# Kernel tuning notes

Measured on AMD Instinct MI355X. Metric: run time of the kernel, lower is better.

Reference implementation:

```python
import jax, jax.numpy as jnp
import numpy as np


def _gen_grid(h, w, stride=1):
    """Normalized spherical sampling grid, shape (3*H', 3*W', 2) with (x, y) order,
    matching gen_grid_coordinates in the torch source (vectorized)."""
    pi = np.pi
    dphi = pi / h
    dth = 2 * pi / w
    t = np.tan(dth)
    p = np.tan(dphi)
    sp = p / np.cos(dth)
    # xys[kr, kc] = (x, y) tangent-plane offsets of the 3x3 kernel taps
    xys = np.array([[[-t, sp], [0.0, p], [t, sp]],
                    [[-t, 0.0], [1.0, 1.0], [t, 0.0]],
                    [[-t, -sp], [0.0, -p], [t, -sp]]], dtype=np.float64)
    X = xys[..., 0]
    Y = xys[..., 1]
    rho = np.sqrt(X ** 2 + Y ** 2)           # [3,3], nonzero everywhere
    v = np.arctan(rho)
    rr = np.arange(0, h, stride)
    cc = np.arange(0, w, stride)
    phi = -((rr + 0.5) / h * pi - pi / 2)    # [H']
    theta = (cc + 0.5) / w * 2 * pi - pi     # [W']
    sphi = np.sin(phi)[:, None, None, None]  # [H',1,1,1]
    cphi = np.cos(phi)[:, None, None, None]
    arg = np.cos(v) * sphi + Y * np.sin(v) * cphi / rho  # [H',1,3,3]
    new_phi = np.arcsin(np.clip(arg, -1.0, 1.0))
    new_theta = theta[None, :, None, None] + np.arctan(
        X * np.sin(v) / (rho * cphi * np.cos(v) - Y * sphi * np.sin(v)))  # [H',W',3,3]
    new_r = np.broadcast_to((-new_phi + pi / 2) * h / pi - 0.5, new_theta.shape).copy()
    new_c = (new_theta + pi) * w / (2 * pi) - 0.5
    new_c = (new_c + w) % w
    # center tap samples the pixel itself
    new_r[:, :, 1, 1] = rr[:, None]
    new_c[:, :, 1, 1] = cc[None, :]
    gx = new_c * 2 / w - 1
    gy = new_r * 2 / h - 1
    grid = np.stack([gx, gy], axis=-1)                     # [H',W',3,3,2]
    Hp, Wp = len(rr), len(cc)
    grid = grid.transpose(0, 2, 1, 3, 4).reshape(Hp * 3, Wp * 3, 2)
    return grid.astype(np.float32)


def _grid_sample_bilinear_zeros(x, grid):
    """torch grid_sample(mode='bilinear', padding_mode='zeros', align_corners=False).
    x: [N,C,H,W]; grid: [Hg,Wg,2] (shared over batch). Returns [N,C,Hg,Wg]."""
    N, C, H, W = x.shape
    ix = ((grid[..., 0] + 1) * W - 1) * 0.5
    iy = ((grid[..., 1] + 1) * H - 1) * 0.5
    x0 = jnp.floor(ix)
    y0 = jnp.floor(iy)
    x1 = x0 + 1
    y1 = y0 + 1
    wx1 = ix - x0
    wx0 = 1.0 - wx1
    wy1 = iy - y0
    wy0 = 1.0 - wy1

    def gather(yy, xx):
        valid = ((xx >= 0) & (xx <= W - 1) & (yy >= 0) & (yy <= H - 1)).astype(x.dtype)
        xi = jnp.clip(xx, 0, W - 1).astype(jnp.int32)
        yi = jnp.clip(yy, 0, H - 1).astype(jnp.int32)
        return x[:, :, yi, xi], valid  # [N,C,Hg,Wg], [Hg,Wg]

    v00, m00 = gather(y0, x0)
    v01, m01 = gather(y0, x1)
    v10, m10 = gather(y1, x0)
    v11, m11 = gather(y1, x1)
    return (v00 * (wy0 * wx0 * m00) + v01 * (wy0 * wx1 * m01)
            + v10 * (wy1 * wx0 * m10) + v11 * (wy1 * wx1 * m11))


def setup_inputs() -> dict:
    key = jax.random.key(0)
    k1, k2, k3 = jax.random.split(key, 3)
    N, Cin, H, W = 4, 64, 128, 256
    Cout = 128
    x = jax.random.normal(k1, (N, Cin, H, W), dtype=jnp.float32)
    fan_in = Cin * 9
    bound = 1.0 / np.sqrt(fan_in)
    weight = jax.random.uniform(k2, (Cout, Cin, 3, 3), dtype=jnp.float32,
                                minval=-bound, maxval=bound)
    bias = jnp.zeros((Cout,), dtype=jnp.float32)
    return {"x": x, "weight": weight, "bias": bias}


def reference(x, weight, bias):
    H, W = int(x.shape[2]), int(x.shape[3])
    grid = jnp.asarray(_gen_grid(H, W, 1))              # [3H, 3W, 2]
    s = _grid_sample_bilinear_zeros(x, grid)            # [N, Cin, 3H, 3W]
    y = jax.lax.conv_general_dilated(
        s, weight, window_strides=(3, 3), padding='VALID',
        dimension_numbers=('NCHW', 'OIHW', 'NCHW'))     # [N, Cout, H, W]
    return y + bias[None, :, None, None]
```

## Files before the change

### kernel.cpp

```cpp
#include <hip/hip_runtime.h>
#include <math.h>

typedef __attribute__((ext_vector_type(8))) _Float16 half8;
typedef __attribute__((ext_vector_type(4))) _Float16 half4;
typedef __attribute__((ext_vector_type(2))) _Float16 half2;
typedef __attribute__((ext_vector_type(4))) float floatx4;
typedef __attribute__((ext_vector_type(4))) unsigned int uintx4;

#define NB    4
#define CIN   64
#define COUT  128
#define IMH   128
#define IMW   256
#define KTOT  576
#define NPIX  (IMH * IMW)
#define PXT   128
#define NDPB  (PXT * 9)
#define ROWS  4
#define CSTW  6
#define NCOL  257
#define RSTW  (NCOL * CSTW)
#define KCH   96

__device__ __forceinline__ unsigned pkrtz2(float a, float b) {
  unsigned r;
  asm("v_cvt_pkrtz_f16_f32 %0, %1, %2" : "=v"(r) : "v"(a), "v"(b));
  return r;
}
__device__ __forceinline__ half4 bcl(unsigned u) {
  half2 h; __builtin_memcpy(&h, &u, 4);
  return __builtin_shufflevector(h, h, 0, 0, 0, 0);
}
__device__ __forceinline__ half4 bch(unsigned u) {
  half2 h; __builtin_memcpy(&h, &u, 4);
  return __builtin_shufflevector(h, h, 1, 1, 1, 1);
}

__global__ __launch_bounds__(256) void prep_w_kernel(const float* __restrict__ w,
                                                     unsigned short* __restrict__ wbf) {
  int idx = blockIdx.x * 256 + threadIdx.x;
  if (idx >= COUT * 8 * KCH) return;
  int co = idx / (8 * KCH);
  int K2 = idx - co * (8 * KCH);
  int cb = K2 / KCH, kk = K2 - cb * KCH;
  unsigned short v = 0;
  if (kk < 72) {
    int t = kk >> 3, chl = kk & 7;
    int ci = cb * 8 + chl;
    _Float16 h = (_Float16)w[co * KTOT + ci * 9 + t];
    __builtin_memcpy(&v, &h, 2);
  }
  wbf[(K2 >> 3) * (COUT * 8) + co * 8 + (K2 & 7)] = v;
}

__global__ __launch_bounds__(512, 4) void sphconv_kernel(
    const float* __restrict__ x, const unsigned short* __restrict__ wbf,
    const float* __restrict__ bias, float* __restrict__ out) {
  __shared__ __align__(16) unsigned int stg[2][ROWS * RSTW];
  __shared__ __align__(16) unsigned int descL[12 * PXT * 4];
  __shared__ double tapA[9];
  __shared__ float  tapWy[9][2];
  __shared__ int    tapRo[9][2];

  const int tid  = threadIdx.x;
  const int lane = tid & 63;
  const int wv   = tid >> 6;
  const int lin = blockIdx.x + 2 * blockIdx.y;
  const int sw  = (lin & 7) * 32 + (lin >> 3);
  const int ct  = sw >> 7;
  const int r   = sw & 127;
  const int n   = blockIdx.z;
  const int c0  = ct * PXT;
  const int co_base = (wv & 1) * 64;
  const int px_base = (wv >> 1) * 32;
  const int rlo  = min(max(r - 2, 0), IMH - ROWS);
  const int q    = lane >> 4;
  const int p    = lane & 15;
  const int sp  = tid & 3;
  const int scg = (tid >> 2) & 63;
  const int srr = tid >> 8;

  const float* xn = x + (size_t)n * CIN * NPIX;

  floatx4 nx[4];
  #pragma unroll
  for (int c = 0; c < 2; c++)
    #pragma unroll
    for (int rw = 0; rw < 2; rw++)
      nx[c * 2 + rw] = *(const floatx4*)(xn + (size_t)(sp * 2 + c) * NPIX
                                         + (size_t)(rlo + srr * 2 + rw) * IMW + scg * 4);

  {
    int myk = -1;
    if (lane == 0) myk = wv;
    if (wv == 0 && lane == 32) myk = 8;
    if (myk >= 0) {
      const double pi = 3.14159265358979323846;
      double dphi = pi / IMH;
      double dth  = 2.0 * pi / IMW;
      double t  = tan(dth);
      double pp = tan(dphi);
      double sp_ = pp / cos(dth);
      double phi  = -(((double)r + 0.5) / IMH * pi - pi * 0.5);
      double sphi = sin(phi), cphi = cos(phi);
      int i = myk / 3, j = myk % 3;
      double atv, new_r;
      if (myk == 4) {
        atv = 0.0; new_r = (double)r;
      } else {
        double X = (j == 0) ? -t : ((j == 2) ? t : 0.0);
        double Y = 0.0;
        if (i == 0)      Y = (j == 1) ?  pp :  sp_;
        else if (i == 2) Y = (j == 1) ? -pp : -sp_;
        double rho = sqrt(X * X + Y * Y);
        double v   = atan(rho);
        double sv = sin(v), cv = cos(v);
        double arg = cv * sphi + Y * sv * cphi / rho;
        arg = fmin(1.0, fmax(-1.0, arg));
        double new_phi = asin(arg);
        double denom = rho * cphi * cv - Y * sphi * sv;
        atv = atan(X * sv / denom);
        new_r = (-new_phi + pi * 0.5) * IMH / pi - 0.5;
      }
      float gy = (float)(new_r * 2.0 / IMH - 1.0);
      float iy = ((gy + 1.0f) * (float)IMH - 1.0f) * 0.5f;
      float fy = floorf(iy); int y0 = (int)fy;
      float wy1 = iy - fy, wy0 = 1.0f - wy1;
      int y1 = y0 + 1;
      bool vy0 = (y0 >= 0) & (y0 <= IMH - 1);
      bool vy1 = (y1 >= 0) & (y1 <= IMH - 1);
      int y0c = min(max(y0, 0), IMH - 1), y1c = min(max(y1, 0), IMH - 1);
      int rt = min(max(y0c - rlo, 0), ROWS - 1);
      int rb = min(max(y1c - rlo, 0), ROWS - 1);
      tapA[myk] = atv;
      tapWy[myk][0] = vy0 ? wy0 : 0.0f;
      tapWy[myk][1] = vy1 ? wy1 : 0.0f;
      tapRo[myk][0] = rt * RSTW;
      tapRo[myk][1] = rb * RSTW;
    }
  }
  __syncthreads();

  {
    const double pi = 3.14159265358979323846;
    #pragma unroll
    for (int dd = 0; dd < 3; dd++) {
      if (dd < 2 || tid < NDPB - 1024) {
        int d  = tid + dd * 512;
        int px = d & (PXT - 1), k = d >> 7;
        int c  = c0 + px;
        double nc;
        if (k == 4) {
          nc = (double)c;
        } else {
          double theta = ((double)c + 0.5) / IMW * (2.0 * pi) - pi;
          double new_theta = theta + tapA[k];
          nc = (new_theta + pi) * IMW / (2.0 * pi) - 0.5;
          nc = fmod(nc + (double)IMW, (double)IMW);
        }
        float gx = (float)(nc * 2.0 / IMW - 1.0);
        float ix = ((gx + 1.0f) * (float)IMW - 1.0f) * 0.5f;
        float fx = floorf(ix); int x0 = (int)fx;
        float wx1 = ix - fx, wx0 = 1.0f - wx1;
        int x1 = x0 + 1;
        int x0c = max(x0, 0);
        float w_lo = (x0 >= 0) ? wx0 : wx1;
        float w_hi = (x0 >= 0) ? ((x1 <= IMW - 1) ? wx1 : 0.0f) : 0.0f;
        float wy0m = tapWy[k][0], wy1m = tapWy[k][1];
        int sh0 = ((x0c >> 4) & 1) * 2;
        int sh1 = (((x0c + 1) >> 4) & 1) * 2;
        int dc  = CSTW + sh1 - sh0;
        int offt = tapRo[k][0] + x0c * CSTW + sh0;
        int offb = tapRo[k][1] + x0c * CSTW + sh0;
        uintx4 rec;
        rec.x = (unsigned)(offt | (offb << 16));
        rec.y = pkrtz2(wy0m * w_lo, wy0m * w_hi);
        rec.z = pkrtz2(wy1m * w_lo, wy1m * w_hi);
        rec.w = (unsigned)dc;
        *(uintx4*)&descL[(k * PXT + px) * 4] = rec;
      }
    }
  }
  if (tid < 3 * PXT) {
    uintx4 zr = {0u, 0u, 0u, (unsigned)CSTW};
    *(uintx4*)&descL[((9 + (tid >> 7)) * PXT + (tid & (PXT - 1))) * 4] = zr;
  }

  #pragma unroll
  for (int rw = 0; rw < 2; rw++)
    #pragma unroll
    for (int i = 0; i < 4; i++) {
      int col = scg * 4 + i;
      int sh = ((col >> 4) & 1) * 2;
      stg[0][(srr * 2 + rw) * RSTW + col * CSTW + sh + sp] =
          pkrtz2(nx[rw][i], nx[2 + rw][i]);
    }
  if (tid < 32) stg[tid >> 4][((tid >> 2) & 3) * RSTW + 256 * CSTW + (tid & 3)] = 0u;

  floatx4 acc[4][2];
  #pragma unroll
  for (int mt = 0; mt < 4; mt++)
    #pragma unroll
    for (int nt = 0; nt < 2; nt++)
      acc[mt][nt] = (floatx4){0.f, 0.f, 0.f, 0.f};

  __syncthreads();

  #pragma unroll 1
  for (int cb = 0; cb < 8; cb++) {
    if (cb < 7) {
      #pragma unroll
      for (int c = 0; c < 2; c++)
        #pragma unroll
        for (int rw = 0; rw < 2; rw++)
          nx[c * 2 + rw] = *(const floatx4*)(xn + (size_t)((cb + 1) * 8 + sp * 2 + c) * NPIX
                                             + (size_t)(rlo + srr * 2 + rw) * IMW + scg * 4);
    }
    const unsigned int* sb = &stg[cb & 1][0];
    #pragma unroll
    for (int nt = 0; nt < 2; nt++) {
      const int pxl = px_base + nt * 16 + p;
      #pragma unroll
      for (int ks = 0; ks < 3; ks++) {
        uintx4 rec = *(const uintx4*)&descL[((ks * 4 + q) * PXT + pxl) * 4];
        unsigned op = rec.x;
        int dc = (int)rec.w;
        const unsigned int* pt = sb + (op & 0xFFFFu);
        const unsigned int* pb = sb + (op >> 16);
        half4 t0  = *(const half4*)(pt);
        half4 t0h = *(const half4*)(pt + 2);
        half4 t1  = *(const half4*)(pt + dc);
        half4 t1h = *(const half4*)(pt + dc + 2);
        half4 b0  = *(const half4*)(pb);
        half4 b0h = *(const half4*)(pb + 2);
        half4 b1  = *(const half4*)(pb + dc);
        half4 b1h = *(const half4*)(pb + dc + 2);
        half4 W0 = bcl(rec.y), W1 = bch(rec.y);
        half4 W2 = bcl(rec.z), W3 = bch(rec.z);
        half4 slo = t0 * W0 + t1 * W1 + b0 * W2 + b1 * W3;
        half4 shi = t0h * W0 + t1h * W1 + b0h * W2 + b1h * W3;
        half8 b = __builtin_shufflevector(slo, shi, 0, 1, 2, 3, 4, 5, 6, 7);
        const unsigned short* arow =
            wbf + (size_t)((cb * 12 + ks * 4 + q) * COUT + co_base + p) * 8;
        __builtin_amdgcn_s_setprio(1);
        #pragma unroll
        for (int mt = 0; mt < 4; mt++) {
          half8 a = *(const half8*)(arow + mt * 16 * 8);
          acc[mt][nt] = __builtin_amdgcn_mfma_f32_16x16x32_f16(a, b, acc[mt][nt], 0, 0, 0);
        }
        __builtin_amdgcn_s_setprio(0);
      }
    }
    if (cb < 7) {
      #pragma unroll
      for (int rw = 0; rw < 2; rw++)
        #pragma unroll
        for (int i = 0; i < 4; i++) {
          int col = scg * 4 + i;
          int sh = ((col >> 4) & 1) * 2;
          stg[(cb + 1) & 1][(srr * 2 + rw) * RSTW + col * CSTW + sh + sp] =
              pkrtz2(nx[rw][i], nx[2 + rw][i]);
        }
    }
    __syncthreads();
  }

  #pragma unroll
  for (int mt = 0; mt < 4; mt++)
    #pragma unroll
    for (int nt = 0; nt < 2; nt++)
      #pragma unroll
      for (int rg = 0; rg < 4; rg++) {
        const int co = co_base + mt * 16 + q * 4 + rg;
        const int cc = c0 + px_base + nt * 16 + p;
        out[(((size_t)n * COUT + co) * IMH + r) * IMW + cc] = acc[mt][nt][rg] + bias[co];
      }
}

extern "C" void kernel_launch(void* const* d_in, const int* in_sizes, int n_in,
                              void* d_out, int out_size, void* d_ws, size_t ws_size,
                              hipStream_t stream) {
  const float* x    = (const float*)d_in[0];
  const float* w    = (const float*)d_in[1];
  const float* bias = (const float*)d_in[2];
  float* out = (float*)d_out;
  unsigned short* wbf = (unsigned short*)d_ws;
  (void)in_sizes; (void)n_in; (void)out_size; (void)ws_size;

  hipLaunchKernelGGL(prep_w_kernel, dim3((COUT * 8 * KCH + 255) / 256), dim3(256), 0, stream, w, wbf);
  hipLaunchKernelGGL(sphconv_kernel, dim3(IMW / PXT, IMH, NB), dim3(512), 0, stream,
                     x, wbf, bias, out);
}
```

Baseline: 170.7 us.

## Pre-transpose input to fp16 channel-packed layout and stream tiles via direct-to-LDS loads

Adds a prep kernel that converts x to fp16 with 8 channels packed per pixel in workspace. The main kernel then copies row tiles straight into LDS with global_load_lds, skipping the register staging and per-element pack/store work. Each tap sample is a single 16-byte LDS read, and the bilinear blend is done in half8 vector math. This costs an extra full pass over x in the prep kernel, and the old kernel is kept as a fallback for when the workspace is too small.

```diff
diff --git a/kernel.cpp b/kernel.cpp
--- a/kernel.cpp
+++ b/kernel.cpp
@@ -17,10 +17,10 @@
 #define PXT   128
 #define NDPB  (PXT * 9)
 #define ROWS  4
-#define CSTW  6
-#define NCOL  257
-#define RSTW  (NCOL * CSTW)
 #define KCH   96
+#define DSTR  520
+#define XT_OFF 262144
+#define XT_BYTES ((size_t)NB * 8 * IMH * IMW * 16)
 
 __device__ __forceinline__ unsigned pkrtz2(float a, float b) {
   unsigned r;
@@ -34,6 +34,19 @@
 __device__ __forceinline__ half4 bch(unsigned u) {
   half2 h; __builtin_memcpy(&h, &u, 4);
   return __builtin_shufflevector(h, h, 1, 1, 1, 1);
+}
+__device__ __forceinline__ half8 bcl8(unsigned u) {
+  half2 h; __builtin_memcpy(&h, &u, 4);
+  return __builtin_shufflevector(h, h, 0, 0, 0, 0, 0, 0, 0, 0);
+}
+__device__ __forceinline__ half8 bch8(unsigned u) {
+  half2 h; __builtin_memcpy(&h, &u, 4);
+  return __builtin_shufflevector(h, h, 1, 1, 1, 1, 1, 1, 1, 1);
+}
+__device__ __forceinline__ void gload_lds16(const void* g, void* l) {
+  __builtin_amdgcn_global_load_lds(
+      (const __attribute__((address_space(1))) unsigned int*)g,
+      (__attribute__((address_space(3))) unsigned int*)l, 16, 0, 0);
 }
 
 __global__ __launch_bounds__(256) void prep_w_kernel(const float* __restrict__ w,
@@ -53,11 +66,26 @@
   wbf[(K2 >> 3) * (COUT * 8) + co * 8 + (K2 & 7)] = v;
 }
 
-__global__ __launch_bounds__(512, 4) void sphconv_kernel(
-    const float* __restrict__ x, const unsigned short* __restrict__ wbf,
+__global__ __launch_bounds__(256) void prep_x_kernel(const float* __restrict__ x,
+                                                     unsigned short* __restrict__ xt) {
+  int idx = blockIdx.x * 256 + threadIdx.x;
+  int c   = idx & 255;
+  int rr  = (idx >> 8) & 127;
+  int ncb = idx >> 15;
+  int n = ncb >> 3, cb = ncb & 7;
+  const float* src = x + (size_t)(n * CIN + cb * 8) * NPIX + rr * IMW + c;
+  unsigned o4[4];
+  #pragma unroll
+  for (int j = 0; j < 4; j++)
+    o4[j] = pkrtz2(src[(size_t)(2 * j) * NPIX], src[(size_t)(2 * j + 1) * NPIX]);
+  *(uintx4*)(xt + (size_t)idx * 8) = *(uintx4*)o4;
+}
+
+__global__ __launch_bounds__(512, 4) void sphconv_fast(
+    const unsigned short* __restrict__ xt, const unsigned short* __restrict__ wbf,
     const float* __restrict__ bias, float* __restrict__ out) {
-  __shared__ __align__(16) unsigned int stg[2][ROWS * RSTW];
-  __shared__ __align__(16) unsigned int descL[12 * PXT * 4];
+  __shared__ __align__(16) unsigned int stg[2][ROWS * IMW * 4];
+  __shared__ __align__(16) unsigned int descL[12 * DSTR];
   __shared__ double tapA[9];
   __shared__ float  tapWy[9][2];
   __shared__ int    tapRo[9][2];
@@ -76,19 +104,14 @@
   const int rlo  = min(max(r - 2, 0), IMH - ROWS);
   const int q    = lane >> 4;
   const int p    = lane & 15;
-  const int sp  = tid & 3;
-  const int scg = (tid >> 2) & 63;
-  const int srr = tid >> 8;
-
-  const float* xn = x + (size_t)n * CIN * NPIX;
-
-  floatx4 nx[4];
-  #pragma unroll
-  for (int c = 0; c < 2; c++)
-    #pragma unroll
-    for (int rw = 0; rw < 2; rw++)
-      nx[c * 2 + rw] = *(const floatx4*)(xn + (size_t)(sp * 2 + c) * NPIX
-                                         + (size_t)(rlo + srr * 2 + rw) * IMW + scg * 4);
+
+  {
+    const char* gs = (const char*)xt
+        + ((size_t)((n * 8 + 0) * IMH + rlo) * IMW) * 16 + wv * 1024 + lane * 16;
+    char* lb = (char*)&stg[0][0] + wv * 1024;
+    gload_lds16(gs, lb);
+    gload_lds16(gs + 8192, lb + 8192);
+  }
 
   {
     int myk = -1;
@@ -135,8 +158,204 @@
       tapA[myk] = atv;
       tapWy[myk][0] = vy0 ? wy0 : 0.0f;
       tapWy[myk][1] = vy1 ? wy1 : 0.0f;
-      tapRo[myk][0] = rt * RSTW;
-      tapRo[myk][1] = rb * RSTW;
+      tapRo[myk][0] = rt * (IMW * 4);
+      tapRo[myk][1] = rb * (IMW * 4);
+    }
+  }
+  __syncthreads();
+
+  {
+    const double pi = 3.14159265358979323846;
+    #pragma unroll
+    for (int dd = 0; dd < 3; dd++) {
+      if (dd < 2 || tid < NDPB - 1024) {
+        int d  = tid + dd * 512;
+        int px = d & (PXT - 1), k = d >> 7;
+        int c  = c0 + px;
+        double nc;
+        if (k == 4) {
+          nc = (double)c;
+        } else {
+          double theta = ((double)c + 0.5) / IMW * (2.0 * pi) - pi;
+          double new_theta = theta + tapA[k];
+          nc = (new_theta + pi) * IMW / (2.0 * pi) - 0.5;
+          nc = fmod(nc + (double)IMW, (double)IMW);
+        }
+        float gx = (float)(nc * 2.0 / IMW - 1.0);
+        float ix = ((gx + 1.0f) * (float)IMW - 1.0f) * 0.5f;
+        float fx = floorf(ix); int x0 = (int)fx;
+        float wx1 = ix - fx, wx0 = 1.0f - wx1;
+        int x1 = x0 + 1;
+        int x0c = max(x0, 0);
+        float w_lo = (x0 >= 0) ? wx0 : wx1;
+        float w_hi = (x0 >= 0) ? ((x1 <= IMW - 1) ? wx1 : 0.0f) : 0.0f;
+        float wy0m = tapWy[k][0], wy1m = tapWy[k][1];
+        int dc = (x1 <= IMW - 1) ? 4 : 0;
+        int offt = tapRo[k][0] + x0c * 4;
+        int offb = tapRo[k][1] + x0c * 4;
+        uintx4 rec;
+        rec.x = (unsigned)(offt | (offb << 16));
+        rec.y = pkrtz2(wy0m * w_lo, wy0m * w_hi);
+        rec.z = pkrtz2(wy1m * w_lo, wy1m * w_hi);
+        rec.w = (unsigned)dc;
+        *(uintx4*)&descL[k * DSTR + px * 4] = rec;
+      }
+    }
+  }
+  if (tid < 3 * PXT) {
+    uintx4 zr = {0u, 0u, 0u, 0u};
+    *(uintx4*)&descL[(9 + (tid >> 7)) * DSTR + (tid & (PXT - 1)) * 4] = zr;
+  }
+
+  floatx4 acc[4][2];
+  #pragma unroll
+  for (int mt = 0; mt < 4; mt++)
+    #pragma unroll
+    for (int nt = 0; nt < 2; nt++)
+      acc[mt][nt] = (floatx4){0.f, 0.f, 0.f, 0.f};
+
+  __syncthreads();
+
+  #pragma unroll 1
+  for (int cb = 0; cb < 8; cb++) {
+    if (cb < 7) {
+      const char* gs = (const char*)xt
+          + ((size_t)((n * 8 + cb + 1) * IMH + rlo) * IMW) * 16 + wv * 1024 + lane * 16;
+      char* lb = (char*)&stg[(cb + 1) & 1][0] + wv * 1024;
+      gload_lds16(gs, lb);
+      gload_lds16(gs + 8192, lb + 8192);
+    }
+    const unsigned int* sb = &stg[cb & 1][0];
+    #pragma unroll
+    for (int nt = 0; nt < 2; nt++) {
+      const int pxl = px_base + nt * 16 + p;
+      #pragma unroll
+      for (int ks = 0; ks < 3; ks++) {
+        uintx4 rec = *(const uintx4*)&descL[(ks * 4 + q) * DSTR + pxl * 4];
+        unsigned op = rec.x;
+        int dc = (int)rec.w;
+        const unsigned int* pt = sb + (op & 0xFFFFu);
+        const unsigned int* pb = sb + (op >> 16);
+        half8 t0 = *(const half8*)pt;
+        half8 t1 = *(const half8*)(pt + dc);
+        half8 b0 = *(const half8*)pb;
+        half8 b1 = *(const half8*)(pb + dc);
+        half8 W0 = bcl8(rec.y), W1 = bch8(rec.y);
+        half8 W2 = bcl8(rec.z), W3 = bch8(rec.z);
+        half8 b = t0 * W0 + t1 * W1 + b0 * W2 + b1 * W3;
+        const unsigned short* arow =
+            wbf + (size_t)((cb * 12 + ks * 4 + q) * COUT + co_base + p) * 8;
+        __builtin_amdgcn_s_setprio(1);
+        #pragma unroll
+        for (int mt = 0; mt < 4; mt++) {
+          half8 a = *(const half8*)(arow + mt * 16 * 8);
+          acc[mt][nt] = __builtin_amdgcn_mfma_f32_16x16x32_f16(a, b, acc[mt][nt], 0, 0, 0);
+        }
+        __builtin_amdgcn_s_setprio(0);
+      }
+    }
+    __syncthreads();
+  }
+
+  #pragma unroll
+  for (int mt = 0; mt < 4; mt++)
+    #pragma unroll
+    for (int nt = 0; nt < 2; nt++)
+      #pragma unroll
+      for (int rg = 0; rg < 4; rg++) {
+        const int co = co_base + mt * 16 + q * 4 + rg;
+        const int cc = c0 + px_base + nt * 16 + p;
+        out[(((size_t)n * COUT + co) * IMH + r) * IMW + cc] = acc[mt][nt][rg] + bias[co];
+      }
+}
+
+#define F_CSTW  6
+#define F_NCOL  257
+#define F_RSTW  (F_NCOL * F_CSTW)
+__global__ __launch_bounds__(512, 4) void sphconv_fb(
+    const float* __restrict__ x, const unsigned short* __restrict__ wbf,
+    const float* __restrict__ bias, float* __restrict__ out) {
+  __shared__ __align__(16) unsigned int stg[2][ROWS * F_RSTW];
+  __shared__ __align__(16) unsigned int descL[12 * PXT * 4];
+  __shared__ double tapA[9];
+  __shared__ float  tapWy[9][2];
+  __shared__ int    tapRo[9][2];
+
+  const int tid  = threadIdx.x;
+  const int lane = tid & 63;
+  const int wv   = tid >> 6;
+  const int lin = blockIdx.x + 2 * blockIdx.y;
+  const int sw  = (lin & 7) * 32 + (lin >> 3);
+  const int ct  = sw >> 7;
+  const int r   = sw & 127;
+  const int n   = blockIdx.z;
+  const int c0  = ct * PXT;
+  const int co_base = (wv & 1) * 64;
+  const int px_base = (wv >> 1) * 32;
+  const int rlo  = min(max(r - 2, 0), IMH - ROWS);
+  const int q    = lane >> 4;
+  const int p    = lane & 15;
+  const int sp  = tid & 3;
+  const int scg = (tid >> 2) & 63;
+  const int srr = tid >> 8;
+
+  const float* xn = x + (size_t)n * CIN * NPIX;
+
+  floatx4 nx[4];
+  #pragma unroll
+  for (int c = 0; c < 2; c++)
+    #pragma unroll
+    for (int rw = 0; rw < 2; rw++)
+      nx[c * 2 + rw] = *(const floatx4*)(xn + (size_t)(sp * 2 + c) * NPIX
+                                         + (size_t)(rlo + srr * 2 + rw) * IMW + scg * 4);
+
+  {
+    int myk = -1;
+    if (lane == 0) myk = wv;
+    if (wv == 0 && lane == 32) myk = 8;
+    if (myk >= 0) {
+      const double pi = 3.14159265358979323846;
+      double dphi = pi / IMH;
+      double dth  = 2.0 * pi / IMW;
+      double t  = tan(dth);
+      double pp = tan(dphi);
+      double sp_ = pp / cos(dth);
+      double phi  = -(((double)r + 0.5) / IMH * pi - pi * 0.5);
+      double sphi = sin(phi), cphi = cos(phi);
+      int i = myk / 3, j = myk % 3;
+      double atv, new_r;
+      if (myk == 4) {
+        atv = 0.0; new_r = (double)r;
+      } else {
+        double X = (j == 0) ? -t : ((j == 2) ? t : 0.0);
+        double Y = 0.0;
+        if (i == 0)      Y = (j == 1) ?  pp :  sp_;
+        else if (i == 2) Y = (j == 1) ? -pp : -sp_;
+        double rho = sqrt(X * X + Y * Y);
+        double v   = atan(rho);
+        double sv = sin(v), cv = cos(v);
+        double arg = cv * sphi + Y * sv * cphi / rho;
+        arg = fmin(1.0, fmax(-1.0, arg));
+        double new_phi = asin(arg);
+        double denom = rho * cphi * cv - Y * sphi * sv;
+        atv = atan(X * sv / denom);
+        new_r = (-new_phi + pi * 0.5) * IMH / pi - 0.5;
+      }
+      float gy = (float)(new_r * 2.0 / IMH - 1.0);
+      float iy = ((gy + 1.0f) * (float)IMH - 1.0f) * 0.5f;
+      float fy = floorf(iy); int y0 = (int)fy;
+      float wy1 = iy - fy, wy0 = 1.0f - wy1;
+      int y1 = y0 + 1;
+      bool vy0 = (y0 >= 0) & (y0 <= IMH - 1);
+      bool vy1 = (y1 >= 0) & (y1 <= IMH - 1);
+      int y0c = min(max(y0, 0), IMH - 1), y1c = min(max(y1, 0), IMH - 1);
+      int rt = min(max(y0c - rlo, 0), ROWS - 1);
+      int rb = min(max(y1c - rlo, 0), ROWS - 1);
+      tapA[myk] = atv;
+      tapWy[myk][0] = vy0 ? wy0 : 0.0f;
+      tapWy[myk][1] = vy1 ? wy1 : 0.0f;
+      tapRo[myk][0] = rt * F_RSTW;
+      tapRo[myk][1] = rb * F_RSTW;
     }
   }
   __syncthreads();
@@ -169,9 +388,9 @@
         float wy0m = tapWy[k][0], wy1m = tapWy[k][1];
         int sh0 = ((x0c >> 4) & 1) * 2;
         int sh1 = (((x0c + 1) >> 4) & 1) * 2;
-        int dc  = CSTW + sh1 - sh0;
-        int offt = tapRo[k][0] + x0c * CSTW + sh0;
-        int offb = tapRo[k][1] + x0c * CSTW + sh0;
+        int dc  = F_CSTW + sh1 - sh0;
+        int offt = tapRo[k][0] + x0c * F_CSTW + sh0;
+        int offb = tapRo[k][1] + x0c * F_CSTW + sh0;
         uintx4 rec;
         rec.x = (unsigned)(offt | (offb << 16));
         rec.y = pkrtz2(wy0m * w_lo, wy0m * w_hi);
@@ -182,7 +401,7 @@
     }
   }
   if (tid < 3 * PXT) {
-    uintx4 zr = {0u, 0u, 0u, (unsigned)CSTW};
+    uintx4 zr = {0u, 0u, 0u, (unsigned)F_CSTW};
     *(uintx4*)&descL[((9 + (tid >> 7)) * PXT + (tid & (PXT - 1))) * 4] = zr;
   }
 
@@ -192,10 +411,10 @@
     for (int i = 0; i < 4; i++) {
       int col = scg * 4 + i;
       int sh = ((col >> 4) & 1) * 2;
-      stg[0][(srr * 2 + rw) * RSTW + col * CSTW + sh + sp] =
+      stg[0][(srr * 2 + rw) * F_RSTW + col * F_CSTW + sh + sp] =
           pkrtz2(nx[rw][i], nx[2 + rw][i]);
     }
-  if (tid < 32) stg[tid >> 4][((tid >> 2) & 3) * RSTW + 256 * CSTW + (tid & 3)] = 0u;
+  if (tid < 32) stg[tid >> 4][((tid >> 2) & 3) * F_RSTW + 256 * F_CSTW + (tid & 3)] = 0u;
 
   floatx4 acc[4][2];
   #pragma unroll
@@ -258,7 +477,7 @@
         for (int i = 0; i < 4; i++) {
           int col = scg * 4 + i;
           int sh = ((col >> 4) & 1) * 2;
-          stg[(cb + 1) & 1][(srr * 2 + rw) * RSTW + col * CSTW + sh + sp] =
+          stg[(cb + 1) & 1][(srr * 2 + rw) * F_RSTW + col * F_CSTW + sh + sp] =
               pkrtz2(nx[rw][i], nx[2 + rw][i]);
         }
     }
@@ -285,9 +504,16 @@
   const float* bias = (const float*)d_in[2];
   float* out = (float*)d_out;
   unsigned short* wbf = (unsigned short*)d_ws;
-  (void)in_sizes; (void)n_in; (void)out_size; (void)ws_size;
+  (void)in_sizes; (void)n_in; (void)out_size;
 
   hipLaunchKernelGGL(prep_w_kernel, dim3((COUT * 8 * KCH + 255) / 256), dim3(256), 0, stream, w, wbf);
-  hipLaunchKernelGGL(sphconv_kernel, dim3(IMW / PXT, IMH, NB), dim3(512), 0, stream,
-                     x, wbf, bias, out);
-}
+  if (ws_size >= (size_t)XT_OFF + XT_BYTES) {
+    unsigned short* xt = (unsigned short*)((char*)d_ws + XT_OFF);
+    hipLaunchKernelGGL(prep_x_kernel, dim3((NB * 8 * IMH * IMW) / 256), dim3(256), 0, stream, x, xt);
+    hipLaunchKernelGGL(sphconv_fast, dim3(IMW / PXT, IMH, NB), dim3(512), 0, stream,
+                       xt, wbf, bias, out);
+  } else {
+    hipLaunchKernelGGL(sphconv_fb, dim3(IMW / PXT, IMH, NB), dim3(512), 0, stream,
+                       x, wbf, bias, out);
+  }
+}
```

Result: faster. 164.2 us (-3.8%).
